# Performance work log

Hardware: AMD Instinct MI355X
Metric: run time of the kernel (lower is better)

Reference implementation:

```python
import jax, jax.numpy as jnp
import numpy as np

HID = 1024
HEADS = 16
HEAD_DIM = HID // HEADS


def setup_inputs() -> dict:
    key = jax.random.key(0)
    ks = jax.random.split(key, 11)
    s = 1.0 / np.sqrt(HID)
    return {
        "query": jax.random.normal(ks[0], (4, 2048, HID), jnp.float32),
        "key": jax.random.normal(ks[1], (4, 2048, HID), jnp.float32),
        "value": jax.random.normal(ks[2], (4, 2048, HID), jnp.float32),
        "wq": jax.random.normal(ks[3], (HID, HID), jnp.float32) * s,
        "bq": jnp.zeros((HID,), jnp.float32),
        "wk": jax.random.normal(ks[4], (HID, HID), jnp.float32) * s,
        "bk": jnp.zeros((HID,), jnp.float32),
        "wv": jax.random.normal(ks[5], (HID, HID), jnp.float32) * s,
        "bv": jnp.zeros((HID,), jnp.float32),
        "wo": jax.random.normal(ks[6], (HID, HID), jnp.float32) * s,
        "bo": jnp.zeros((HID,), jnp.float32),
    }


def reference(query, key, value, wq, bq, wk, bk, wv, bv, wo, bo):
    b, s, _ = query.shape
    scale = jnp.sqrt(jnp.asarray(HEAD_DIM, query.dtype))
    # linear projections; weights stored as [in, out]
    Q = (query @ wq + bq).reshape(b, s, HEADS, HEAD_DIM).transpose(0, 2, 1, 3)
    K = (key @ wk + bk).reshape(b, s, HEADS, HEAD_DIM).transpose(0, 2, 1, 3)
    V = (value @ wv + bv).reshape(b, s, HEADS, HEAD_DIM).transpose(0, 2, 1, 3)
    energy = jnp.einsum('bhqd,bhkd->bhqk', Q, K) / scale  # [B,H,S,S]
    attention = jax.nn.softmax(energy, axis=-1)  # dropout p=0 -> identity
    x = jnp.einsum('bhqk,bhkd->bhqd', attention, V)
    x = x.transpose(0, 2, 1, 3).reshape(b, s, HID)
    return x @ wo + bo
```

## Files before the change

kernel.cpp:

```cpp
#include <hip/hip_runtime.h>
#include <hip/hip_bf16.h>

#define B_   4
#define S_   2048
#define HID_ 1024
#define H_   16
#define D_   64
#define M_   (B_ * S_)

typedef __attribute__((ext_vector_type(8)))  short bf16x8;
typedef __attribute__((ext_vector_type(4)))  float f32x4;
typedef __attribute__((ext_vector_type(16))) float f32x16;

#define GAS __attribute__((address_space(1)))
#define LAS __attribute__((address_space(3)))

__device__ __forceinline__ unsigned short f2bf(float f) {
    union { float f; unsigned int u; } x; x.f = f;
    unsigned int u = x.u;
    return (unsigned short)((u + 0x7fffu + ((u >> 16) & 1u)) >> 16);
}

__global__ __launch_bounds__(256)
void cast3(const float* __restrict__ q, const float* __restrict__ k, const float* __restrict__ v,
           unsigned short* __restrict__ oq, unsigned short* __restrict__ ok,
           unsigned short* __restrict__ ov) {
    const int sel = blockIdx.x >> 12;
    const int i = (blockIdx.x & 4095) * 256 + threadIdx.x;
    const float* in = (sel == 0) ? q : (sel == 1) ? k : v;
    unsigned short* out = (sel == 0) ? oq : (sel == 1) ? ok : ov;
    const f32x4 a = ((const f32x4*)in)[i * 2];
    const f32x4 b = ((const f32x4*)in)[i * 2 + 1];
    bf16x8 w;
#pragma unroll
    for (int j = 0; j < 4; j++) { w[j] = (short)f2bf(a[j]); w[4 + j] = (short)f2bf(b[j]); }
    ((bf16x8*)out)[i] = w;
}

__global__ void transpose_cast(const float* __restrict__ w0, const float* __restrict__ w1,
                               const float* __restrict__ w2, const float* __restrict__ w3,
                               unsigned short* __restrict__ o0, unsigned short* __restrict__ o1,
                               unsigned short* __restrict__ o2, unsigned short* __restrict__ o3) {
    __shared__ float t[32][33];
    const float* w = (blockIdx.z == 0) ? w0 : (blockIdx.z == 1) ? w1 : (blockIdx.z == 2) ? w2 : w3;
    unsigned short* o = (blockIdx.z == 0) ? o0 : (blockIdx.z == 1) ? o1 : (blockIdx.z == 2) ? o2 : o3;
    const int tx = threadIdx.x, ty = threadIdx.y;
    const int bx = blockIdx.x * 32, by = blockIdx.y * 32;
#pragma unroll
    for (int i = 0; i < 4; i++)
        t[ty + i * 8][tx] = w[(size_t)(by + ty + i * 8) * HID_ + bx + tx];
    __syncthreads();
#pragma unroll
    for (int i = 0; i < 4; i++)
        o[(size_t)(bx + ty + i * 8) * HID_ + by + tx] = f2bf(t[tx][ty + i * 8]);
}

__global__ __launch_bounds__(256, 3)
void gemm_qkv(const unsigned short* __restrict__ aq, const unsigned short* __restrict__ ak,
              const unsigned short* __restrict__ av, const unsigned short* __restrict__ wqkvT,
              const float* __restrict__ bq, const float* __restrict__ bk,
              const float* __restrict__ bv, unsigned short* __restrict__ Qp,
              unsigned short* __restrict__ Kp, unsigned short* __restrict__ Vt, float cvt) {
    constexpr int BK = 32;
    __shared__ unsigned short smem[8704];
    unsigned short* As = smem;
    unsigned short* Bs = smem + 4096;

    const int tid  = threadIdx.x;
    const int lane = tid & 63;
    const int wave = tid >> 6;
    const int quad = lane >> 4;
    const int col  = lane & 15;
    const int wr   = (wave & 1) * 64;
    const int wc   = (wave >> 1) * 64;
    const int m0   = blockIdx.x * 128;
    const int third = blockIdx.y >> 3;
    const int n0l   = (blockIdx.y & 7) * 128;
    const bool vmode = (third == 2);

    const unsigned short* act = (third == 0) ? aq : (third == 1) ? ak : av;
    const float* bias = (third == 0) ? bq : (third == 1) ? bk : bv;
    unsigned short* outp = (third == 0) ? Qp : (third == 1) ? Kp : Vt;
    const float oscale = (third == 0) ? cvt : 1.f;

    const int grow = wave * 16 + (lane >> 2);
    const int gcol = (lane & 3) * 8;
    const unsigned short* wgp = wqkvT + (size_t)(third * HID_ + n0l + grow) * HID_ + gcol;
    const unsigned short* agp = act + (size_t)(m0 + grow) * HID_ + gcol;
    const unsigned short* rgp = vmode ? agp : wgp;
    const unsigned short* cgp = vmode ? wgp : agp;
    unsigned short* asb = &As[wave * 512];
    unsigned short* bsb = &Bs[wave * 512];

    f32x4 zero; zero[0] = 0.f; zero[1] = 0.f; zero[2] = 0.f; zero[3] = 0.f;
    f32x4 acc[4][4];
#pragma unroll
    for (int ri = 0; ri < 4; ri++)
#pragma unroll
        for (int ci = 0; ci < 4; ci++) acc[ri][ci] = zero;

    for (int kt = 0; kt < HID_; kt += BK) {
        __builtin_amdgcn_global_load_lds((const GAS unsigned int*)(rgp + kt),
                                         (LAS unsigned int*)asb, 16, 0, 0);
        __builtin_amdgcn_global_load_lds((const GAS unsigned int*)(rgp + kt + (size_t)64 * HID_),
                                         (LAS unsigned int*)(asb + 2048), 16, 0, 0);
        __builtin_amdgcn_global_load_lds((const GAS unsigned int*)(cgp + kt),
                                         (LAS unsigned int*)bsb, 16, 0, 0);
        __builtin_amdgcn_global_load_lds((const GAS unsigned int*)(cgp + kt + (size_t)64 * HID_),
                                         (LAS unsigned int*)(bsb + 2048), 16, 0, 0);
        __syncthreads();

        bf16x8 af[4], cf[4];
#pragma unroll
        for (int i = 0; i < 4; i++) af[i] = *(const bf16x8*)&As[(wr + i * 16 + col) * BK + quad * 8];
#pragma unroll
        for (int i = 0; i < 4; i++) cf[i] = *(const bf16x8*)&Bs[(wc + i * 16 + col) * BK + quad * 8];
#pragma unroll
        for (int ri = 0; ri < 4; ri++)
#pragma unroll
            for (int ci = 0; ci < 4; ci++)
                acc[ri][ci] = __builtin_amdgcn_mfma_f32_16x16x32_bf16(af[ri], cf[ci], acc[ri][ci], 0, 0, 0);
        __syncthreads();
    }

    unsigned short* RB = smem;
#pragma unroll
    for (int ph = 0; ph < 2; ph++) {
        if ((wave >> 1) == ph) {
#pragma unroll
            for (int ri = 0; ri < 4; ri++) {
                f32x4 bv4;
                if (!vmode) bv4 = *(const f32x4*)&bias[n0l + wr + ri * 16 + quad * 4];
#pragma unroll
                for (int ci = 0; ci < 4; ci++) {
                    float b0, b1, b2, b3;
                    if (!vmode) { b0 = bv4[0]; b1 = bv4[1]; b2 = bv4[2]; b3 = bv4[3]; }
                    else { b0 = b1 = b2 = b3 = bias[n0l + wc + ci * 16 + col]; }
                    const unsigned int u0 = f2bf((acc[ri][ci][0] + b0) * oscale);
                    const unsigned int u1 = f2bf((acc[ri][ci][1] + b1) * oscale);
                    const unsigned int u2 = f2bf((acc[ri][ci][2] + b2) * oscale);
                    const unsigned int u3 = f2bf((acc[ri][ci][3] + b3) * oscale);
                    uint2 w; w.x = u0 | (u1 << 16); w.y = u2 | (u3 << 16);
                    *(uint2*)&RB[(ci * 16 + col) * 136 + wr + ri * 16 + quad * 4] = w;
                }
            }
        }
        __syncthreads();
#pragma unroll
        for (int it = 0; it < 4; it++) {
            const int c   = it * 256 + tid;
            const int row = c >> 4, ch = c & 15;
            const bf16x8 v = *(const bf16x8*)&RB[row * 136 + ch * 8];
            if (!vmode) {
                const int n = n0l + ch * 8;
                const int h = n >> 6, d = n & 63;
                const int m = m0 + ph * 64 + row;
                *(bf16x8*)&outp[(((size_t)(m >> 11) * H_ + h) * S_ + (m & 2047)) * D_ + d] = v;
            } else {
                const int m = m0 + ch * 8;
                const int n = n0l + ph * 64 + row;
                const int h = n >> 6, d = n & 63;
                *(bf16x8*)&outp[(((size_t)(m >> 11) * H_ + h) * D_ + d) * S_ + (m & 2047)] = v;
            }
        }
        __syncthreads();
    }
}

__global__ __launch_bounds__(256, 3)
void gemm_o(const unsigned short* __restrict__ A, const unsigned short* __restrict__ Bt,
            const float* __restrict__ bias, float* __restrict__ outp) {
    constexpr int BK = 32;
    __shared__ float smemf[64 * 132];
    unsigned short* As = (unsigned short*)smemf;
    unsigned short* Bs = As + 4096;

    const int tid  = threadIdx.x;
    const int lane = tid & 63;
    const int wave = tid >> 6;
    const int quad = lane >> 4;
    const int col  = lane & 15;
    const int wn   = (wave >> 1) * 64;
    const int wm   = (wave & 1) * 64;
    const int m0   = blockIdx.x * 128;
    const int n0l  = blockIdx.y * 128;

    const int grow = wave * 16 + (lane >> 2);
    const int gcol = (lane & 3) * 8;
    const unsigned short* agp = A + (size_t)(m0 + grow) * HID_ + gcol;
    const unsigned short* wgp = Bt + (size_t)(n0l + grow) * HID_ + gcol;
    unsigned short* asb = &As[wave * 512];
    unsigned short* bsb = &Bs[wave * 512];

    f32x4 zero; zero[0] = 0.f; zero[1] = 0.f; zero[2] = 0.f; zero[3] = 0.f;
    f32x4 acc[4][4];
#pragma unroll
    for (int ri = 0; ri < 4; ri++)
#pragma unroll
        for (int ci = 0; ci < 4; ci++) acc[ri][ci] = zero;

    for (int kt = 0; kt < HID_; kt += BK) {
        __builtin_amdgcn_global_load_lds((const GAS unsigned int*)(wgp + kt),
                                         (LAS unsigned int*)asb, 16, 0, 0);
        __builtin_amdgcn_global_load_lds((const GAS unsigned int*)(wgp + kt + (size_t)64 * HID_),
                                         (LAS unsigned int*)(asb + 2048), 16, 0, 0);
        __builtin_amdgcn_global_load_lds((const GAS unsigned int*)(agp + kt),
                                         (LAS unsigned int*)bsb, 16, 0, 0);
        __builtin_amdgcn_global_load_lds((const GAS unsigned int*)(agp + kt + (size_t)64 * HID_),
                                         (LAS unsigned int*)(bsb + 2048), 16, 0, 0);
        __syncthreads();

        bf16x8 wf[4], af[4];
#pragma unroll
        for (int i = 0; i < 4; i++) wf[i] = *(const bf16x8*)&As[(wn + i * 16 + col) * BK + quad * 8];
#pragma unroll
        for (int i = 0; i < 4; i++) af[i] = *(const bf16x8*)&Bs[(wm + i * 16 + col) * BK + quad * 8];
#pragma unroll
        for (int ri = 0; ri < 4; ri++)
#pragma unroll
            for (int ci = 0; ci < 4; ci++)
                acc[ri][ci] = __builtin_amdgcn_mfma_f32_16x16x32_bf16(wf[ri], af[ci], acc[ri][ci], 0, 0, 0);
        __syncthreads();
    }

#pragma unroll
    for (int ph = 0; ph < 2; ph++) {
        if ((wave & 1) == ph) {
#pragma unroll
            for (int ri = 0; ri < 4; ri++) {
                const f32x4 bv4 = *(const f32x4*)&bias[n0l + wn + ri * 16 + quad * 4];
#pragma unroll
                for (int ci = 0; ci < 4; ci++) {
                    f32x4 v;
#pragma unroll
                    for (int i = 0; i < 4; i++) v[i] = acc[ri][ci][i] + bv4[i];
                    *(f32x4*)&smemf[(ci * 16 + col) * 132 + wn + ri * 16 + quad * 4] = v;
                }
            }
        }
        __syncthreads();
#pragma unroll
        for (int it = 0; it < 8; it++) {
            const int c   = it * 256 + tid;
            const int row = c >> 5, ch = c & 31;
            const f32x4 v = *(const f32x4*)&smemf[row * 132 + ch * 4];
            *(f32x4*)&outp[(size_t)(m0 + ph * 64 + row) * HID_ + n0l + ch * 4] = v;
        }
        __syncthreads();
    }
}

__global__ __launch_bounds__(256, 4)
void attn_k(const unsigned short* __restrict__ Qp, const unsigned short* __restrict__ Kp,
            const unsigned short* __restrict__ Vt, unsigned short* __restrict__ Xc) {
    constexpr int LT = 72;
    constexpr int NT = S_ / 64;
    __shared__ unsigned short Ks[2][64 * LT];
    __shared__ unsigned short Vs[2][64 * LT];

    const int tid  = threadIdx.x;
    const int lane = tid & 63;
    const int wave = tid >> 6;
    const int l31  = lane & 31;
    const int hw   = lane >> 5;
    const int bh   = blockIdx.y;
    const int q0   = blockIdx.x * 128 + wave * 32;

    const unsigned short* Qb = Qp + (size_t)bh * S_ * D_;
    const unsigned short* Kb = Kp + (size_t)bh * S_ * D_;
    const unsigned short* Vb = Vt + (size_t)bh * D_ * S_;

    bf16x8 qf[4];
#pragma unroll
    for (int ks = 0; ks < 4; ks++)
        qf[ks] = *(const bf16x8*)&Qb[(q0 + l31) * D_ + ks * 16 + hw * 8];

    f32x16 o[2];
#pragma unroll
    for (int t = 0; t < 2; t++)
#pragma unroll
        for (int i = 0; i < 16; i++) o[t][i] = 0.f;
    float lpart = 0.f;

    const int srow = tid >> 3;
    const int seg  = (tid & 7) * 8;
    bf16x8 kr[2], vr[2];

#pragma unroll
    for (int it = 0; it < 2; it++) {
        const int row = it * 32 + srow;
        kr[it] = *(const bf16x8*)&Kb[(size_t)row * D_ + seg];
        vr[it] = *(const bf16x8*)&Vb[(size_t)row * S_ + seg];
    }
#pragma unroll
    for (int it = 0; it < 2; it++) {
        const int row = it * 32 + srow;
        *(bf16x8*)&Ks[0][row * LT + seg] = kr[it];
        *(bf16x8*)&Vs[0][row * LT + seg] = vr[it];
    }
#pragma unroll
    for (int it = 0; it < 2; it++) {
        const int row = it * 32 + srow;
        kr[it] = *(const bf16x8*)&Kb[(size_t)(64 + row) * D_ + seg];
        vr[it] = *(const bf16x8*)&Vb[(size_t)row * S_ + 64 + seg];
    }
    __syncthreads();

    for (int t = 0; t < NT; ++t) {
        const int cur = t & 1;
#pragma unroll
        for (int g = 0; g < 2; g++) {
            f32x16 e;
#pragma unroll
            for (int i = 0; i < 16; i++) e[i] = 0.f;
#pragma unroll
            for (int ks = 0; ks < 4; ks++) {
                const bf16x8 a = *(const bf16x8*)&Ks[cur][(g * 32 + l31) * LT + ks * 16 + hw * 8];
                e = __builtin_amdgcn_mfma_f32_32x32x16_bf16(a, qf[ks], e, 0, 0, 0);
            }
            unsigned int ulo[4], uhi[4];
#pragma unroll
            for (int grp = 0; grp < 4; grp++) {
                const float p0 = __builtin_amdgcn_exp2f(e[grp * 4 + 0]);
                const float p1 = __builtin_amdgcn_exp2f(e[grp * 4 + 1]);
                const float p2 = __builtin_amdgcn_exp2f(e[grp * 4 + 2]);
                const float p3 = __builtin_amdgcn_exp2f(e[grp * 4 + 3]);
                lpart += (p0 + p1) + (p2 + p3);
                asm("v_cvt_pk_bf16_f32 %0, %1, %2" : "=v"(ulo[grp]) : "v"(p0), "v"(p1));
                asm("v_cvt_pk_bf16_f32 %0, %1, %2" : "=v"(uhi[grp]) : "v"(p2), "v"(p3));
            }
#pragma unroll
            for (int sub = 0; sub < 2; sub++) {
                unsigned int w0 = ulo[2 * sub], w2 = ulo[2 * sub + 1];
                unsigned int w1 = uhi[2 * sub], w3 = uhi[2 * sub + 1];
                asm("v_permlane32_swap_b32 %0, %1" : "+v"(w0), "+v"(w2));
                asm("v_permlane32_swap_b32 %0, %1" : "+v"(w1), "+v"(w3));
                union { unsigned int u[4]; bf16x8 v; } pf;
                pf.u[0] = w0; pf.u[1] = w1; pf.u[2] = w2; pf.u[3] = w3;
                const int ks = g * 2 + sub;
#pragma unroll
                for (int tt = 0; tt < 2; tt++) {
                    const bf16x8 vf = *(const bf16x8*)&Vs[cur][(tt * 32 + l31) * LT + ks * 16 + hw * 8];
                    o[tt] = __builtin_amdgcn_mfma_f32_32x32x16_bf16(vf, pf.v, o[tt], 0, 0, 0);
                }
            }
        }

        if (t + 1 < NT) {
#pragma unroll
            for (int it = 0; it < 2; it++) {
                const int row = it * 32 + srow;
                *(bf16x8*)&Ks[cur ^ 1][row * LT + seg] = kr[it];
                *(bf16x8*)&Vs[cur ^ 1][row * LT + seg] = vr[it];
            }
            if (t + 2 < NT) {
                const int c0 = (t + 2) * 64;
#pragma unroll
                for (int it = 0; it < 2; it++) {
                    const int row = it * 32 + srow;
                    kr[it] = *(const bf16x8*)&Kb[(size_t)(c0 + row) * D_ + seg];
                    vr[it] = *(const bf16x8*)&Vb[(size_t)row * S_ + c0 + seg];
                }
            }
        }
        __syncthreads();
    }

    float l = lpart;
    l += __shfl_xor(l, 32);
    const float inv = 1.f / l;

    const int b = bh >> 4, h = bh & 15;
    const int s = q0 + l31;
    unsigned short* xp = &Xc[((size_t)(b * S_ + s)) * HID_ + h * D_];
#pragma unroll
    for (int t = 0; t < 2; t++)
#pragma unroll
        for (int grp = 0; grp < 4; grp++) {
            const unsigned int u0 = f2bf(o[t][grp * 4 + 0] * inv);
            const unsigned int u1 = f2bf(o[t][grp * 4 + 1] * inv);
            const unsigned int u2 = f2bf(o[t][grp * 4 + 2] * inv);
            const unsigned int u3 = f2bf(o[t][grp * 4 + 3] * inv);
            uint2 w; w.x = u0 | (u1 << 16); w.y = u2 | (u3 << 16);
            *(uint2*)&xp[t * 32 + grp * 8 + hw * 4] = w;
        }
}

extern "C" void kernel_launch(void* const* d_in, const int* in_sizes, int n_in,
                              void* d_out, int out_size, void* d_ws, size_t ws_size,
                              hipStream_t stream) {
    (void)in_sizes; (void)n_in; (void)out_size; (void)ws_size;
    const float* query = (const float*)d_in[0];
    const float* key   = (const float*)d_in[1];
    const float* value = (const float*)d_in[2];
    const float* wq    = (const float*)d_in[3];
    const float* bq    = (const float*)d_in[4];
    const float* wk    = (const float*)d_in[5];
    const float* bk    = (const float*)d_in[6];
    const float* wv    = (const float*)d_in[7];
    const float* bv    = (const float*)d_in[8];
    const float* wo    = (const float*)d_in[9];
    const float* bo    = (const float*)d_in[10];
    float* out = (float*)d_out;

    unsigned short* ws  = (unsigned short*)d_ws;
    const size_t WSZ = (size_t)HID_ * HID_;
    const size_t TSZ = (size_t)M_ * HID_;
    unsigned short* wqkvT = ws;
    unsigned short* woT = ws + 3 * WSZ;
    unsigned short* Qp  = woT + WSZ;
    unsigned short* Kp  = Qp + TSZ;
    unsigned short* Vt  = Kp + TSZ;
    unsigned short* Xc  = Vt + TSZ;
    unsigned short* Xb  = Xc + TSZ;

    const float cvt = 0.125f * 1.44269504f;

    transpose_cast<<<dim3(32, 32, 4), dim3(32, 8), 0, stream>>>(
        wq, wk, wv, wo, wqkvT, wqkvT + WSZ, wqkvT + 2 * WSZ, woT);

    cast3<<<3 * 4096, 256, 0, stream>>>(query, key, value, Xc, Xb, Xb + TSZ);

    gemm_qkv<<<dim3(M_ / 128, 24), 256, 0, stream>>>(
        Xc, Xb, Xb + TSZ, wqkvT, bq, bk, bv, Qp, Kp, Vt, cvt);

    attn_k<<<dim3(S_ / 128, B_ * H_), 256, 0, stream>>>(Qp, Kp, Vt, Xc);

    gemm_o<<<dim3(M_ / 128, 8), 256, 0, stream>>>(Xc, woT, bo, out);
}
```

Before: 350.7 us.

## Double-buffer LDS tiles in QKV and output projection GEMMs

```diff
diff --git a/kernel.cpp b/kernel.cpp
--- a/kernel.cpp
+++ b/kernel.cpp
@@ -55,16 +55,15 @@
         o[(size_t)(bx + ty + i * 8) * HID_ + by + tx] = f2bf(t[tx][ty + i * 8]);
 }
 
-__global__ __launch_bounds__(256, 3)
+__global__ __launch_bounds__(256, 4)
 void gemm_qkv(const unsigned short* __restrict__ aq, const unsigned short* __restrict__ ak,
               const unsigned short* __restrict__ av, const unsigned short* __restrict__ wqkvT,
               const float* __restrict__ bq, const float* __restrict__ bk,
               const float* __restrict__ bv, unsigned short* __restrict__ Qp,
               unsigned short* __restrict__ Kp, unsigned short* __restrict__ Vt, float cvt) {
     constexpr int BK = 32;
-    __shared__ unsigned short smem[8704];
-    unsigned short* As = smem;
-    unsigned short* Bs = smem + 4096;
+    constexpr int NT = HID_ / BK;
+    __shared__ unsigned short smem[2][8192];
 
     const int tid  = threadIdx.x;
     const int lane = tid & 63;
@@ -89,8 +88,19 @@
     const unsigned short* agp = act + (size_t)(m0 + grow) * HID_ + gcol;
     const unsigned short* rgp = vmode ? agp : wgp;
     const unsigned short* cgp = vmode ? wgp : agp;
-    unsigned short* asb = &As[wave * 512];
-    unsigned short* bsb = &Bs[wave * 512];
+
+    auto stage = [&](int buf, int kt) {
+        unsigned short* as_ = &smem[buf][wave * 512];
+        unsigned short* bs_ = &smem[buf][4096 + wave * 512];
+        __builtin_amdgcn_global_load_lds((const GAS unsigned int*)(rgp + kt),
+                                         (LAS unsigned int*)as_, 16, 0, 0);
+        __builtin_amdgcn_global_load_lds((const GAS unsigned int*)(rgp + kt + (size_t)64 * HID_),
+                                         (LAS unsigned int*)(as_ + 2048), 16, 0, 0);
+        __builtin_amdgcn_global_load_lds((const GAS unsigned int*)(cgp + kt),
+                                         (LAS unsigned int*)bs_, 16, 0, 0);
+        __builtin_amdgcn_global_load_lds((const GAS unsigned int*)(cgp + kt + (size_t)64 * HID_),
+                                         (LAS unsigned int*)(bs_ + 2048), 16, 0, 0);
+    };
 
     f32x4 zero; zero[0] = 0.f; zero[1] = 0.f; zero[2] = 0.f; zero[3] = 0.f;
     f32x4 acc[4][4];
@@ -99,22 +109,19 @@
 #pragma unroll
         for (int ci = 0; ci < 4; ci++) acc[ri][ci] = zero;
 
-    for (int kt = 0; kt < HID_; kt += BK) {
-        __builtin_amdgcn_global_load_lds((const GAS unsigned int*)(rgp + kt),
-                                         (LAS unsigned int*)asb, 16, 0, 0);
-        __builtin_amdgcn_global_load_lds((const GAS unsigned int*)(rgp + kt + (size_t)64 * HID_),
-                                         (LAS unsigned int*)(asb + 2048), 16, 0, 0);
-        __builtin_amdgcn_global_load_lds((const GAS unsigned int*)(cgp + kt),
-                                         (LAS unsigned int*)bsb, 16, 0, 0);
-        __builtin_amdgcn_global_load_lds((const GAS unsigned int*)(cgp + kt + (size_t)64 * HID_),
-                                         (LAS unsigned int*)(bsb + 2048), 16, 0, 0);
-        __syncthreads();
-
+    stage(0, 0);
+    __syncthreads();
+
+    for (int t = 0; t < NT; ++t) {
+        const int cur = t & 1;
+        if (t + 1 < NT) stage(cur ^ 1, (t + 1) * BK);
+        const unsigned short* Asc = smem[cur];
+        const unsigned short* Bsc = smem[cur] + 4096;
         bf16x8 af[4], cf[4];
 #pragma unroll
-        for (int i = 0; i < 4; i++) af[i] = *(const bf16x8*)&As[(wr + i * 16 + col) * BK + quad * 8];
-#pragma unroll
-        for (int i = 0; i < 4; i++) cf[i] = *(const bf16x8*)&Bs[(wc + i * 16 + col) * BK + quad * 8];
+        for (int i = 0; i < 4; i++) af[i] = *(const bf16x8*)&Asc[(wr + i * 16 + col) * BK + quad * 8];
+#pragma unroll
+        for (int i = 0; i < 4; i++) cf[i] = *(const bf16x8*)&Bsc[(wc + i * 16 + col) * BK + quad * 8];
 #pragma unroll
         for (int ri = 0; ri < 4; ri++)
 #pragma unroll
@@ -123,7 +130,7 @@
         __syncthreads();
     }
 
-    unsigned short* RB = smem;
+    unsigned short* RB = &smem[0][0];
 #pragma unroll
     for (int ph = 0; ph < 2; ph++) {
         if ((wave >> 1) == ph) {
@@ -167,13 +174,13 @@
     }
 }
 
-__global__ __launch_bounds__(256, 3)
+__global__ __launch_bounds__(256, 4)
 void gemm_o(const unsigned short* __restrict__ A, const unsigned short* __restrict__ Bt,
             const float* __restrict__ bias, float* __restrict__ outp) {
     constexpr int BK = 32;
+    constexpr int NT = HID_ / BK;
     __shared__ float smemf[64 * 132];
-    unsigned short* As = (unsigned short*)smemf;
-    unsigned short* Bs = As + 4096;
+    unsigned short* sb = (unsigned short*)smemf;
 
     const int tid  = threadIdx.x;
     const int lane = tid & 63;
@@ -189,8 +196,19 @@
     const int gcol = (lane & 3) * 8;
     const unsigned short* agp = A + (size_t)(m0 + grow) * HID_ + gcol;
     const unsigned short* wgp = Bt + (size_t)(n0l + grow) * HID_ + gcol;
-    unsigned short* asb = &As[wave * 512];
-    unsigned short* bsb = &Bs[wave * 512];
+
+    auto stage = [&](int buf, int kt) {
+        unsigned short* as_ = sb + buf * 8192 + wave * 512;
+        unsigned short* bs_ = sb + buf * 8192 + 4096 + wave * 512;
+        __builtin_amdgcn_global_load_lds((const GAS unsigned int*)(wgp + kt),
+                                         (LAS unsigned int*)as_, 16, 0, 0);
+        __builtin_amdgcn_global_load_lds((const GAS unsigned int*)(wgp + kt + (size_t)64 * HID_),
+                                         (LAS unsigned int*)(as_ + 2048), 16, 0, 0);
+        __builtin_amdgcn_global_load_lds((const GAS unsigned int*)(agp + kt),
+                                         (LAS unsigned int*)bs_, 16, 0, 0);
+        __builtin_amdgcn_global_load_lds((const GAS unsigned int*)(agp + kt + (size_t)64 * HID_),
+                                         (LAS unsigned int*)(bs_ + 2048), 16, 0, 0);
+    };
 
     f32x4 zero; zero[0] = 0.f; zero[1] = 0.f; zero[2] = 0.f; zero[3] = 0.f;
     f32x4 acc[4][4];
@@ -199,22 +217,19 @@
 #pragma unroll
         for (int ci = 0; ci < 4; ci++) acc[ri][ci] = zero;
 
-    for (int kt = 0; kt < HID_; kt += BK) {
-        __builtin_amdgcn_global_load_lds((const GAS unsigned int*)(wgp + kt),
-                                         (LAS unsigned int*)asb, 16, 0, 0);
-        __builtin_amdgcn_global_load_lds((const GAS unsigned int*)(wgp + kt + (size_t)64 * HID_),
-                                         (LAS unsigned int*)(asb + 2048), 16, 0, 0);
-        __builtin_amdgcn_global_load_lds((const GAS unsigned int*)(agp + kt),
-                                         (LAS unsigned int*)bsb, 16, 0, 0);
-        __builtin_amdgcn_global_load_lds((const GAS unsigned int*)(agp + kt + (size_t)64 * HID_),
-                                         (LAS unsigned int*)(bsb + 2048), 16, 0, 0);
-        __syncthreads();
-
+    stage(0, 0);
+    __syncthreads();
+
+    for (int t = 0; t < NT; ++t) {
+        const int cur = t & 1;
+        if (t + 1 < NT) stage(cur ^ 1, (t + 1) * BK);
+        const unsigned short* Asc = sb + cur * 8192;
+        const unsigned short* Bsc = Asc + 4096;
         bf16x8 wf[4], af[4];
 #pragma unroll
-        for (int i = 0; i < 4; i++) wf[i] = *(const bf16x8*)&As[(wn + i * 16 + col) * BK + quad * 8];
-#pragma unroll
-        for (int i = 0; i < 4; i++) af[i] = *(const bf16x8*)&Bs[(wm + i * 16 + col) * BK + quad * 8];
+        for (int i = 0; i < 4; i++) wf[i] = *(const bf16x8*)&Asc[(wn + i * 16 + col) * BK + quad * 8];
+#pragma unroll
+        for (int i = 0; i < 4; i++) af[i] = *(const bf16x8*)&Bsc[(wm + i * 16 + col) * BK + quad * 8];
 #pragma unroll
         for (int ri = 0; ri < 4; ri++)
 #pragma unroll
```

Measured after the change: 337.9 us. 1.04x faster.
